# Kernel optimization log

Measured on AMD Instinct MI355X. Metric: run time of the kernel, lower is better.

The kernel has to match this reference:

```python
import jax, jax.numpy as jnp
import numpy as np

N = 1024   # chain length n
B = 4      # bond_dim (forced by eye(4) bias in original)
P = 2      # phys_dim
BS = 8     # batch size


def setup_inputs() -> dict:
    key = jax.random.key(0)
    k1, k2, k3 = jax.random.split(key, 3)
    data = jax.random.randint(k1, (BS, N), 0, 2).astype(jnp.float32)
    # near-identity init (identity + small noise), as in the original (std*randn + eye bias),
    # but with std large enough to be numerically non-trivial yet stable over ~n matmuls
    eye_b = jnp.eye(B, dtype=jnp.float32)[:, :, None]            # (B, B, 1) broadcast over phys
    tri_up = 0.01 * jax.random.normal(k2, ((N - 1) * N // 2, B, B, P), jnp.float32) + eye_b
    diag = 0.01 * jax.random.normal(k3, (N, B, P), jnp.float32) + 1.0
    return {"data": data, "tri_up": tri_up, "diag": diag}


def reference(data, tri_up, diag):
    bs, n = data.shape
    b = tri_up.shape[1]
    p = tri_up.shape[3]
    emb = jnp.stack([data, 1.0 - data], axis=2)                  # (bs, n, p)
    # scatter tri_up into lower triangle (incl. diagonal) of (n-1, n-1) grid
    r, c = jnp.tril_indices(n - 1)
    T = jnp.zeros((n - 1, n - 1, b, b, p), tri_up.dtype).at[r, c].set(tri_up)
    # contract physical index with embedded spins of sites 0..n-2; output axes swapped to (m, n, bs, b, b)
    T = jnp.einsum('nmlri,bmi->mnblr', T, emb[:, :-1])           # (n-1, n-1, bs, b, b)
    # strict lower triangle (m > n) -> identity matrices
    ru, cu = jnp.triu_indices(n - 1, k=1)
    T = T.at[cu, ru].set(jnp.eye(b, dtype=T.dtype))
    # binary-tree contraction along axis 0 (recursive doubling of 4x4 matmuls)
    size = T.shape[0]
    while size > 1:
        half = size // 2
        nice = 2 * half
        leftover = T[nice:]
        T = jnp.einsum('mnbik,mnbkj->mnbij', T[0:nice:2], T[1:nice:2])
        T = jnp.concatenate([T, leftover], axis=0)
        size = half + (size % 2)
    T = T[0][..., 0, :]                                          # (n-1, bs, b): first row of each matrix
    out = jnp.einsum('nbd,ndp->nbp', T, diag[1:])                # (n-1, bs, p)
    first = jnp.broadcast_to(diag[0, 0], out[0].shape)[None]     # (1, bs, p)
    out = jnp.concatenate([first, out], axis=0)                  # (n, bs, p)
    logx = jax.nn.log_softmax(out, axis=-1).transpose(1, 0, 2)   # (bs, n, p)
    log_prob = logx[:, :, 0] * data + logx[:, :, 1] * (1.0 - data)
    return log_prob.sum(-1)                                      # (bs,)
```

## Files before the change

### kernel.cpp

```cpp
#include <hip/hip_runtime.h>


#define NPOS   1024
#define BATCH  8
#define SEGLEN 128
#define MAXSEG 8
#define CH     16
#define NTASK  4600
#define TRI_ELEMS (523776 * 32)

template<int l>
__device__ __forceinline__ float qb(float x) {
    constexpr int ctrl = l * 0x55;
    return __int_as_float(__builtin_amdgcn_update_dpp(
        __float_as_int(x), __float_as_int(x), ctrl, 0xF, 0xF, false));
}
template<int ctrl>
__device__ __forceinline__ float qperm(float x) {
    return __int_as_float(__builtin_amdgcn_update_dpp(
        __float_as_int(x), __float_as_int(x), ctrl, 0xF, 0xF, false));
}

__device__ __forceinline__ void gl_lds16(const float* g, float* l) {
    __builtin_amdgcn_global_load_lds(
        (const __attribute__((address_space(1))) void*)g,
        (__attribute__((address_space(3))) void*)l, 16, 0, 0);
}

#define WAITVM(N) __builtin_amdgcn_s_waitcnt((N) | 0x0F70)

__global__ __launch_bounds__(256, 6) void amps_seg(
        const float* __restrict__ data,
        const float* __restrict__ tri,
        float* __restrict__ segout)
{
    const int tid  = threadIdx.x;
    const int wid  = tid >> 6;
    const int lane = tid & 63;
    const int id   = blockIdx.x * 4 + wid;

    int s = 0, base = 0, cnt = 1023;
    while (id >= base + cnt) { base += cnt; s++; cnt -= 128; }
    const int n  = 1022 - (id - base);
    const int g0 = s * SEGLEN;
    const int steps = min(SEGLEN, n + 1 - g0);

    const int b   = lane >> 3;
    const int sub = lane & 7;
    const int i2  = (lane >> 2) & 1;
    const int j   = lane & 3;

    __shared__ float lds_all[4][3 * CH * 32];
    float* __restrict__ lds = &lds_all[wid][0];

    const int tstart = (n * (n + 1) / 2 + g0) * 32;
    const int full = steps >> 4;
    const int rem  = steps & 15;

    auto stage = [&](int cc, int bufoff) {
        int o0 = min(tstart + cc * 512 + lane * 4,       TRI_ELEMS - 4);
        int o1 = min(tstart + cc * 512 + 256 + lane * 4, TRI_ELEMS - 4);
        gl_lds16(tri + o0, lds + bufoff);
        gl_lds16(tri + o1, lds + bufoff + 256);
    };

    stage(0, 0);
    stage(1, 512);

    unsigned mask[4];
    {
        const float4* dp4 = (const float4*)(data + b * NPOS + g0 + sub * 16);
        float4 q0 = dp4[0], q1 = dp4[1], q2 = dp4[2], q3 = dp4[3];
        float dv[16] = { q0.x,q0.y,q0.z,q0.w, q1.x,q1.y,q1.z,q1.w,
                         q2.x,q2.y,q2.z,q2.w, q3.x,q3.y,q3.z,q3.w };
        unsigned piece = 0;
        #pragma unroll
        for (int t = 0; t < 16; t++)
            piece |= (dv[t] != 1.0f) ? (1u << t) : 0u;
        #pragma unroll
        for (int w = 0; w < 4; w++) {
            unsigned lo = (unsigned)__shfl((int)piece, b * 8 + 2 * w);
            unsigned hi = (unsigned)__shfl((int)piece, b * 8 + 2 * w + 1);
            mask[w] = lo | (hi << 16);
        }
    }

    float c_lo = (i2     == j) ? 1.0f : 0.0f;
    float c_hi = (i2 + 2 == j) ? 1.0f : 0.0f;

    auto compute = [&](int bufoff, unsigned bits, int msteps) {
        const int bj = bufoff + j * 2;
        #pragma unroll
        for (int m = 0; m < CH; m++) {
            if (m >= msteps) break;
            int bi = bj + m * 32 + ((bits >> m) & 1u);
            float t0 = lds[bi],      t1 = lds[bi + 8];
            float t2 = lds[bi + 16], t3 = lds[bi + 24];
            float nl = qb<0>(c_lo) * t0;
            nl = fmaf(qb<1>(c_lo), t1, nl);
            nl = fmaf(qb<2>(c_lo), t2, nl);
            nl = fmaf(qb<3>(c_lo), t3, nl);
            float nh = qb<0>(c_hi) * t0;
            nh = fmaf(qb<1>(c_hi), t1, nh);
            nh = fmaf(qb<2>(c_hi), t2, nh);
            nh = fmaf(qb<3>(c_hi), t3, nh);
            c_lo = nl; c_hi = nh;
        }
    };

    auto bits_of = [&](int cc) -> unsigned {
        return mask[cc >> 1] >> ((cc & 1) * 16);
    };

    int bc = 0, bn = 512, bn2 = 1024;
    for (int c = 0; c < full; c++) {
        stage(c + 2, bn2);
        WAITVM(4);
        compute(bc, bits_of(c), CH);
        int t = bc; bc = bn; bn = bn2; bn2 = t;
    }
    if (rem) {
        WAITVM(0);
        compute(bc, bits_of(full), rem);
    }

    const size_t o = (((size_t)n * MAXSEG + s) * BATCH + b) * 16;
    segout[o + i2 * 4 + j]       = c_lo;
    segout[o + (i2 + 2) * 4 + j] = c_hi;
}

__global__ __launch_bounds__(256) void amps_combine(
        const float* __restrict__ segout,
        const float* __restrict__ diag,
        const float* __restrict__ data,
        float* __restrict__ out)
{
    const int tid = threadIdx.x;
    const int q   = tid >> 5;
    const int sub = tid & 31;
    const int b   = sub >> 2;
    const int r   = sub & 3;
    const int n   = blockIdx.x * 8 + q;

    __shared__ float sh[64];

    float res = 0.0f;
    if (n < NPOS - 1) {
        const int nseg = n / SEGLEN + 1;
        float v = (r == 0) ? 1.0f : 0.0f;
        for (int s2 = 0; s2 < nseg; s2++) {
            const float* p = segout + (((size_t)n * MAXSEG + s2) * BATCH + b) * 16 + r;
            float p0 = p[0], p1 = p[4], p2 = p[8], p3 = p[12];
            float acc = qb<0>(v) * p0;
            acc = fmaf(qb<1>(v), p1, acc);
            acc = fmaf(qb<2>(v), p2, acc);
            v   = fmaf(qb<3>(v), p3, acc);
        }
        const int pos = n + 1;
        const float* dg = diag + pos * 8 + r * 2;
        float o0 = v * dg[0];
        float o1 = v * dg[1];
        o0 += qperm<0xB1>(o0); o0 += qperm<0x4E>(o0);
        o1 += qperm<0xB1>(o1); o1 += qperm<0x4E>(o1);
        float mx  = fmaxf(o0, o1);
        float lse = mx + __logf(__expf(o0 - mx) + __expf(o1 - mx));
        float dsel = data[b * NPOS + pos];
        res = ((dsel == 1.0f) ? o0 : o1) - lse;
    }
    if (r == 0) sh[q * 8 + b] = res;
    __syncthreads();
    if (tid < 8) {
        float ssum = 0.0f;
        #pragma unroll
        for (int qq = 0; qq < 8; qq++) ssum += sh[qq * 8 + tid];
        if (blockIdx.x == 0) {
            float o0 = diag[0], o1 = diag[1];
            float mx  = fmaxf(o0, o1);
            float lse = mx + __logf(__expf(o0 - mx) + __expf(o1 - mx));
            float d0  = data[tid * NPOS];
            ssum += ((d0 == 1.0f) ? o0 : o1) - lse;
        }
        atomicAdd(out + tid, ssum);
    }
}

extern "C" void kernel_launch(void* const* d_in, const int* in_sizes, int n_in,
                              void* d_out, int out_size, void* d_ws, size_t ws_size,
                              hipStream_t stream)
{
    const float* data = (const float*)d_in[0];
    const float* tri  = (const float*)d_in[1];
    const float* diag = (const float*)d_in[2];

    float* segout = (float*)d_ws;
    float* out    = (float*)d_out;

    hipMemsetAsync(d_out, 0, 8 * sizeof(float), stream);
    amps_seg<<<dim3(NTASK / 4), dim3(256), 0, stream>>>(data, tri, segout);
    amps_combine<<<dim3(128), dim3(256), 0, stream>>>(segout, diag, data, out);
}
```

Before: 120.7 us.

## Pack two segment tasks per wave with full-row state and deeper LDS pipeline

The segment kernel now runs one wave per block, and each wave carries two chain-segment tasks, one per half-wave. Each lane holds a full 4-element row state and updates it with plain FMAs from LDS, which removes the DPP broadcasts. Tiles are staged in chunks of 8 steps through a 4-deep async global-to-LDS ring. Partial tail chunks are padded with identity matrices so the loop has no remainder branch. The combine kernel preloads all segment matrices as float4 and selects on the segment count instead of looping a variable number of times. The cost is more LDS traffic per step (16 reads per lane versus 4) and idle work on the shorter task of each pair, in exchange for shorter dependency chains and fewer cross-lane ops.

```diff
diff --git a/kernel.cpp b/kernel.cpp
--- a/kernel.cpp
+++ b/kernel.cpp
@@ -2,11 +2,11 @@
 
 
 #define NPOS   1024
-#define BATCH  8
 #define SEGLEN 128
 #define MAXSEG 8
-#define CH     16
-#define NTASK  4600
+#define CH     8
+#define NBUF   4
+#define NWAVE  2300
 #define TRI_ELEMS (523776 * 32)
 
 template<int l>
@@ -29,104 +29,120 @@
 
 #define WAITVM(N) __builtin_amdgcn_s_waitcnt((N) | 0x0F70)
 
-__global__ __launch_bounds__(256, 6) void amps_seg(
+__device__ __forceinline__ void decode_task(int id, int& s, int& n) {
+    int base = 0, cnt = 1023;
+    s = 0;
+    while (id >= base + cnt) { base += cnt; s++; cnt -= 128; }
+    n = 1022 - (id - base);
+}
+
+__global__ __launch_bounds__(64) void amps_seg(
         const float* __restrict__ data,
         const float* __restrict__ tri,
         float* __restrict__ segout)
 {
-    const int tid  = threadIdx.x;
-    const int wid  = tid >> 6;
-    const int lane = tid & 63;
-    const int id   = blockIdx.x * 4 + wid;
-
-    int s = 0, base = 0, cnt = 1023;
-    while (id >= base + cnt) { base += cnt; s++; cnt -= 128; }
-    const int n  = 1022 - (id - base);
-    const int g0 = s * SEGLEN;
-    const int steps = min(SEGLEN, n + 1 - g0);
-
-    const int b   = lane >> 3;
-    const int sub = lane & 7;
-    const int i2  = (lane >> 2) & 1;
-    const int j   = lane & 3;
-
-    __shared__ float lds_all[4][3 * CH * 32];
-    float* __restrict__ lds = &lds_all[wid][0];
-
-    const int tstart = (n * (n + 1) / 2 + g0) * 32;
-    const int full = steps >> 4;
-    const int rem  = steps & 15;
-
-    auto stage = [&](int cc, int bufoff) {
-        int o0 = min(tstart + cc * 512 + lane * 4,       TRI_ELEMS - 4);
-        int o1 = min(tstart + cc * 512 + 256 + lane * 4, TRI_ELEMS - 4);
-        gl_lds16(tri + o0, lds + bufoff);
-        gl_lds16(tri + o1, lds + bufoff + 256);
+    const int lane = threadIdx.x;
+    const int w    = blockIdx.x;
+    const int t    = lane >> 5;
+    const int q    = lane & 31;
+    const int b    = q >> 2;
+    const int i    = q & 3;
+
+    int sA, nA, sB, nB;
+    decode_task(2 * w,     sA, nA);
+    decode_task(2 * w + 1, sB, nB);
+    const int g0A = sA * SEGLEN,            g0B = sB * SEGLEN;
+    const int stepsA = min(SEGLEN, nA + 1 - g0A);
+    const int stepsB = min(SEGLEN, nB + 1 - g0B);
+    const int tstA = (nA * (nA + 1) / 2 + g0A) * 32;
+    const int tstB = (nB * (nB + 1) / 2 + g0B) * 32;
+
+    const int nchA = (stepsA >> 3) + ((stepsA & 7) ? 1 : 0);
+    const int nchB = (stepsB >> 3) + ((stepsB & 7) ? 1 : 0);
+    const int nch  = max(nchA, nchB);
+
+    const int g0_my    = t ? g0B : g0A;
+    const int steps_my = t ? stepsB : stepsA;
+    const int chunkf   = steps_my >> 3;
+    const int rem      = steps_my & 7;
+    const int n_my     = t ? nB : nA;
+    const int s_my     = t ? sB : sA;
+
+    __shared__ float lds[2][NBUF * CH * 32];
+
+    unsigned m0, m1, m2, m3;
+    {
+        const float4* dp4 =
+            (const float4*)(data + b * NPOS + g0_my + i * 32);
+        float4 f[8];
+        #pragma unroll
+        for (int u = 0; u < 8; u++) f[u] = dp4[u];
+        unsigned piece = 0;
+        #pragma unroll
+        for (int u = 0; u < 8; u++) {
+            piece |= (f[u].x != 1.0f) ? (1u << (u * 4 + 0)) : 0u;
+            piece |= (f[u].y != 1.0f) ? (1u << (u * 4 + 1)) : 0u;
+            piece |= (f[u].z != 1.0f) ? (1u << (u * 4 + 2)) : 0u;
+            piece |= (f[u].w != 1.0f) ? (1u << (u * 4 + 3)) : 0u;
+        }
+        m0 = (unsigned)__shfl((int)piece, t * 32 + b * 4 + 0);
+        m1 = (unsigned)__shfl((int)piece, t * 32 + b * 4 + 1);
+        m2 = (unsigned)__shfl((int)piece, t * 32 + b * 4 + 2);
+        m3 = (unsigned)__shfl((int)piece, t * 32 + b * 4 + 3);
+    }
+
+    auto stageA = [&](int c) {
+        int off = min(tstA + c * 256 + lane * 4, TRI_ELEMS - 4);
+        gl_lds16(tri + off, &lds[0][(c & (NBUF - 1)) * 256]);
     };
-
-    stage(0, 0);
-    stage(1, 512);
-
-    unsigned mask[4];
-    {
-        const float4* dp4 = (const float4*)(data + b * NPOS + g0 + sub * 16);
-        float4 q0 = dp4[0], q1 = dp4[1], q2 = dp4[2], q3 = dp4[3];
-        float dv[16] = { q0.x,q0.y,q0.z,q0.w, q1.x,q1.y,q1.z,q1.w,
-                         q2.x,q2.y,q2.z,q2.w, q3.x,q3.y,q3.z,q3.w };
-        unsigned piece = 0;
-        #pragma unroll
-        for (int t = 0; t < 16; t++)
-            piece |= (dv[t] != 1.0f) ? (1u << t) : 0u;
-        #pragma unroll
-        for (int w = 0; w < 4; w++) {
-            unsigned lo = (unsigned)__shfl((int)piece, b * 8 + 2 * w);
-            unsigned hi = (unsigned)__shfl((int)piece, b * 8 + 2 * w + 1);
-            mask[w] = lo | (hi << 16);
-        }
-    }
-
-    float c_lo = (i2     == j) ? 1.0f : 0.0f;
-    float c_hi = (i2 + 2 == j) ? 1.0f : 0.0f;
-
-    auto compute = [&](int bufoff, unsigned bits, int msteps) {
-        const int bj = bufoff + j * 2;
+    auto stageB = [&](int c) {
+        int off = min(tstB + c * 256 + lane * 4, TRI_ELEMS - 4);
+        gl_lds16(tri + off, &lds[1][(c & (NBUF - 1)) * 256]);
+    };
+
+    stageA(0); stageB(0);
+    stageA(1); stageB(1);
+    stageA(2); stageB(2);
+
+    float* __restrict__ mybuf = &lds[t][0];
+
+    float c0 = (i == 0) ? 1.0f : 0.0f;
+    float c1 = (i == 1) ? 1.0f : 0.0f;
+    float c2 = (i == 2) ? 1.0f : 0.0f;
+    float c3 = (i == 3) ? 1.0f : 0.0f;
+
+    const float idval = ((q >> 3) == ((q >> 1) & 3)) ? 1.0f : 0.0f;
+
+    for (int c = 0; c < nch; c++) {
+        stageA(c + 3); stageB(c + 3);
+        WAITVM(6);
+
+        if (c >= chunkf) {
+            const int mstart = (c == chunkf) ? rem : 0;
+            float* bp = mybuf + (c & (NBUF - 1)) * 256 + q;
+            for (int m = mstart; m < CH; m++) bp[m * 32] = idval;
+        }
+
+        unsigned word = (c < 8) ? ((c < 4) ? m0 : m1) : ((c < 12) ? m2 : m3);
+        const unsigned bits = (word >> ((c & 3) * 8)) & 0xFFu;
+        const float* __restrict__ buf = mybuf + (c & (NBUF - 1)) * 256;
+
         #pragma unroll
         for (int m = 0; m < CH; m++) {
-            if (m >= msteps) break;
-            int bi = bj + m * 32 + ((bits >> m) & 1u);
-            float t0 = lds[bi],      t1 = lds[bi + 8];
-            float t2 = lds[bi + 16], t3 = lds[bi + 24];
-            float nl = qb<0>(c_lo) * t0;
-            nl = fmaf(qb<1>(c_lo), t1, nl);
-            nl = fmaf(qb<2>(c_lo), t2, nl);
-            nl = fmaf(qb<3>(c_lo), t3, nl);
-            float nh = qb<0>(c_hi) * t0;
-            nh = fmaf(qb<1>(c_hi), t1, nh);
-            nh = fmaf(qb<2>(c_hi), t2, nh);
-            nh = fmaf(qb<3>(c_hi), t3, nh);
-            c_lo = nl; c_hi = nh;
-        }
-    };
-
-    auto bits_of = [&](int cc) -> unsigned {
-        return mask[cc >> 1] >> ((cc & 1) * 16);
-    };
-
-    int bc = 0, bn = 512, bn2 = 1024;
-    for (int c = 0; c < full; c++) {
-        stage(c + 2, bn2);
-        WAITVM(4);
-        compute(bc, bits_of(c), CH);
-        int t = bc; bc = bn; bn = bn2; bn2 = t;
-    }
-    if (rem) {
-        WAITVM(0);
-        compute(bc, bits_of(full), rem);
-    }
-
-    const size_t o = (((size_t)n * MAXSEG + s) * BATCH + b) * 16;
-    segout[o + i2 * 4 + j]       = c_lo;
-    segout[o + (i2 + 2) * 4 + j] = c_hi;
+            const float* p = buf + m * 32 + ((bits >> m) & 1u);
+            float n0 = fmaf(c3, p[24], fmaf(c2, p[16], fmaf(c1, p[8],  c0 * p[0])));
+            float n1 = fmaf(c3, p[26], fmaf(c2, p[18], fmaf(c1, p[10], c0 * p[2])));
+            float n2 = fmaf(c3, p[28], fmaf(c2, p[20], fmaf(c1, p[12], c0 * p[4])));
+            float n3 = fmaf(c3, p[30], fmaf(c2, p[22], fmaf(c1, p[14], c0 * p[6])));
+            c0 = n0; c1 = n1; c2 = n2; c3 = n3;
+        }
+    }
+
+    const size_t o = (((size_t)n_my * MAXSEG + s_my) * 8 + b) * 16 + i;
+    segout[o +  0] = c0;
+    segout[o +  4] = c1;
+    segout[o +  8] = c2;
+    segout[o + 12] = c3;
 }
 
 __global__ __launch_bounds__(256) void amps_combine(
@@ -147,15 +163,23 @@
     float res = 0.0f;
     if (n < NPOS - 1) {
         const int nseg = n / SEGLEN + 1;
+        const float* basep = segout + (size_t)n * (MAXSEG * 128)
+                           + b * 16 + r * 4;
+        float4 P[8];
+        #pragma unroll
+        for (int s2 = 0; s2 < 8; s2++)
+            P[s2] = *(const float4*)(basep + s2 * 128);
+
         float v = (r == 0) ? 1.0f : 0.0f;
-        for (int s2 = 0; s2 < nseg; s2++) {
-            const float* p = segout + (((size_t)n * MAXSEG + s2) * BATCH + b) * 16 + r;
-            float p0 = p[0], p1 = p[4], p2 = p[8], p3 = p[12];
-            float acc = qb<0>(v) * p0;
-            acc = fmaf(qb<1>(v), p1, acc);
-            acc = fmaf(qb<2>(v), p2, acc);
-            v   = fmaf(qb<3>(v), p3, acc);
-        }
+        #pragma unroll
+        for (int s2 = 0; s2 < 8; s2++) {
+            float acc = qb<0>(v) * P[s2].x;
+            acc = fmaf(qb<1>(v), P[s2].y, acc);
+            acc = fmaf(qb<2>(v), P[s2].z, acc);
+            float vn = fmaf(qb<3>(v), P[s2].w, acc);
+            v = (s2 < nseg) ? vn : v;
+        }
+
         const int pos = n + 1;
         const float* dg = diag + pos * 8 + r * 2;
         float o0 = v * dg[0];
@@ -196,6 +220,6 @@
     float* out    = (float*)d_out;
 
     hipMemsetAsync(d_out, 0, 8 * sizeof(float), stream);
-    amps_seg<<<dim3(NTASK / 4), dim3(256), 0, stream>>>(data, tri, segout);
+    amps_seg<<<dim3(NWAVE), dim3(64), 0, stream>>>(data, tri, segout);
     amps_combine<<<dim3(128), dim3(256), 0, stream>>>(segout, diag, data, out);
 }
```

Result: no change. 118.9 us (-1.4%).
